# Performance work log

Hardware: AMD Instinct MI355X
Metric: run time of the kernel (lower is better)

Reference implementation:

```python
import jax, jax.numpy as jnp
import numpy as np

EPS = 1e-5

def _layer_norm(x, w, b):
    mu = jnp.mean(x, axis=-1, keepdims=True)
    var = jnp.mean(jnp.square(x - mu), axis=-1, keepdims=True)
    return (x - mu) * jax.lax.rsqrt(var + EPS) * w + b

def setup_inputs() -> dict:
    key = jax.random.key(0)
    ks = jax.random.split(key, 5)
    B, S, C = 1, 512, 128
    scale = 1.0 / np.sqrt(C)
    return {
        "z_ij": jax.random.normal(ks[0], (B, S, S, C), dtype=jnp.float32),
        "ln_w": jnp.ones((C,), jnp.float32),
        "ln_b": jnp.zeros((C,), jnp.float32),
        "wa": jax.random.normal(ks[1], (C, C), dtype=jnp.float32) * scale,
        "wb": jax.random.normal(ks[2], (C, C), dtype=jnp.float32) * scale,
        "wg": jax.random.normal(ks[3], (C, C), dtype=jnp.float32) * scale,
        "fln_w": jnp.ones((C,), jnp.float32),
        "fln_b": jnp.zeros((C,), jnp.float32),
        "wf": jax.random.normal(ks[4], (C, C), dtype=jnp.float32) * scale,
    }

def reference(z_ij, ln_w, ln_b, wa, wb, wg, fln_w, fln_b, wf):
    # z_ij: (B, S, S, C). torch Linear(x) == x @ W.T
    z = _layer_norm(z_ij, ln_w, ln_b)
    a = jax.nn.sigmoid(z @ wa.T)  # (B, S, S, C)
    b = jax.nn.sigmoid(z @ wb.T)
    g = jax.nn.sigmoid(z @ wg.T)
    # torch: einsum('...kic,...kjc->...ijc', a.transpose(-3,-2), b)
    # == out[i,j,c] = sum_k a[i,k,c] * b[k,j,c]
    p = jnp.einsum('bikc,bkjc->bijc', a, b)
    return g * (_layer_norm(p, fln_w, fln_b) @ wf.T)
```

## Files before the change

kernel.cpp:

```cpp
#include <hip/hip_runtime.h>

#define SS 512
#define CC 128
#define RR (SS*SS)

typedef unsigned short u16;
typedef unsigned int   u32;
typedef __attribute__((ext_vector_type(4))) float f32x4;
typedef __attribute__((ext_vector_type(8))) short s16x8;
typedef __attribute__((ext_vector_type(4))) u32   u32x4;

__device__ __forceinline__ float bf2f(u16 u){ u32 x = ((u32)u)<<16; float f; __builtin_memcpy(&f,&x,4); return f; }
__device__ __forceinline__ float sigf(float x){ return 1.f/(1.f + __expf(-x)); }

__device__ __forceinline__ u32 cvtpk(float lo, float hi){
  u32 r; asm("v_cvt_pk_bf16_f32 %0, %1, %2" : "=v"(r) : "v"(lo), "v"(hi)); return r;
}

typedef __attribute__((address_space(1))) void* gptr_t;
typedef __attribute__((address_space(3))) void* lptr_t;
__device__ __forceinline__ void load_lds16(const void* g, void* l){
  __builtin_amdgcn_global_load_lds((gptr_t)(g), (lptr_t)(l), 16, 0, 0);
}

__global__ void k0(const float* __restrict__ wa, const float* __restrict__ wb,
                   const float* __restrict__ wg, u16* __restrict__ wabg)
{
  int t = blockIdx.x*256 + threadIdx.x;
  const float* srcs[3] = {wa, wb, wg};
  int m = t >> 11;
  int e = (t & 2047) * 8;
  const float* s = srcs[m] + e;
  u32 pk[4];
  #pragma unroll
  for (int v=0; v<2; v++){
    f32x4 x = *reinterpret_cast<const f32x4*>(s + v*4);
    pk[v*2]   = cvtpk(x[0], x[1]);
    pk[v*2+1] = cvtpk(x[2], x[3]);
  }
  *reinterpret_cast<u32x4*>(wabg + m*16384 + e) = *reinterpret_cast<u32x4*>(pk);
}

__global__ __launch_bounds__(256,3) void k1(
    const float* __restrict__ z, const float* __restrict__ lnw, const float* __restrict__ lnb,
    const u16* __restrict__ wabg,
    u16* __restrict__ a_t, u16* __restrict__ b_t, u16* __restrict__ g_out,
    float* __restrict__ SaPart)
{
  __shared__ __align__(16) u16 zn[64][136];
  __shared__ __align__(16) u16 wk[64*128];
  __shared__ __align__(16) u16 tr[128*72];
  const int tid = threadIdx.x;
  const int r0  = blockIdx.x * 64;
  const int lane = tid & 63, w = tid >> 6;
  const int iI   = r0 >> 9;
  const int kblk = (r0 >> 6) & 7;

  auto stageW = [&](int m, int h){
    const u16* Wb = wabg + m*16384 + h*8192;
    #pragma unroll
    for (int s=0;s<4;s++){
      int lr = s*16 + (tid>>4);
      const u16* gsrc = Wb + lr*128 + (((tid&15) ^ (lr&7))<<3);
      load_lds16((const void*)gsrc, (void*)&wk[s*2048 + w*512]);
    }
  };

  stageW(0,0);

  {
    int row = tid >> 2, q = tid & 3;
    const float* src = z + (size_t)(r0+row)*CC + q*32;
    float v[32]; float s = 0.f, s2 = 0.f;
    #pragma unroll
    for (int i=0;i<8;i++){
      f32x4 t = *reinterpret_cast<const f32x4*>(src + i*4);
      #pragma unroll
      for (int e=0;e<4;e++){ float x = t[e]; v[i*4+e]=x; s += x; s2 += x*x; }
    }
    s  += __shfl_xor(s,1);  s2 += __shfl_xor(s2,1);
    s  += __shfl_xor(s,2);  s2 += __shfl_xor(s2,2);
    float mu  = s * (1.f/128.f);
    float var = s2*(1.f/128.f) - mu*mu;
    float rs  = rsqrtf(var + 1e-5f);
    #pragma unroll
    for (int i=0;i<4;i++){
      u32 pk[4];
      #pragma unroll
      for (int e=0;e<8;e+=2){
        int ci = i*8+e; int c = q*32 + ci;
        float y0 = (v[ci]  -mu)*rs*lnw[c]   + lnb[c];
        float y1 = (v[ci+1]-mu)*rs*lnw[c+1] + lnb[c+1];
        pk[e>>1] = cvtpk(y0, y1);
      }
      *reinterpret_cast<u32x4*>(&zn[row][q*32 + i*8]) = *reinterpret_cast<u32x4*>(pk);
    }
  }
  __syncthreads();

  s16x8 af[4];
  #pragma unroll
  for (int ks=0;ks<4;ks++)
    af[ks] = *reinterpret_cast<const s16x8*>(&zn[w*16 + (lane&15)][ks*32 + (lane>>4)*8]);

  for (int m=0;m<3;m++){
    f32x4 acc[8];
    #pragma unroll
    for (int cb=0;cb<8;cb++) acc[cb] = (f32x4){0.f,0.f,0.f,0.f};

    #pragma unroll
    for (int cb=0;cb<4;cb++){
      int lr = cb*16 + (lane&15);
      const int rx = (lr&7)<<3;
      const u16* base = &wk[lr*128];
      s16x8 b0 = *reinterpret_cast<const s16x8*>(&base[(  0 + (lane>>4)*8) ^ rx]);
      s16x8 b1 = *reinterpret_cast<const s16x8*>(&base[( 32 + (lane>>4)*8) ^ rx]);
      s16x8 b2 = *reinterpret_cast<const s16x8*>(&base[( 64 + (lane>>4)*8) ^ rx]);
      s16x8 b3 = *reinterpret_cast<const s16x8*>(&base[( 96 + (lane>>4)*8) ^ rx]);
      acc[cb] = __builtin_amdgcn_mfma_f32_16x16x32_bf16(af[0], b0, acc[cb], 0,0,0);
      acc[cb] = __builtin_amdgcn_mfma_f32_16x16x32_bf16(af[1], b1, acc[cb], 0,0,0);
      acc[cb] = __builtin_amdgcn_mfma_f32_16x16x32_bf16(af[2], b2, acc[cb], 0,0,0);
      acc[cb] = __builtin_amdgcn_mfma_f32_16x16x32_bf16(af[3], b3, acc[cb], 0,0,0);
    }
    __syncthreads();
    stageW(m,1);
    __syncthreads();

    #pragma unroll
    for (int cb=4;cb<8;cb++){
      int lr = (cb-4)*16 + (lane&15);
      const int rx = (lr&7)<<3;
      const u16* base = &wk[lr*128];
      s16x8 b0 = *reinterpret_cast<const s16x8*>(&base[(  0 + (lane>>4)*8) ^ rx]);
      s16x8 b1 = *reinterpret_cast<const s16x8*>(&base[( 32 + (lane>>4)*8) ^ rx]);
      s16x8 b2 = *reinterpret_cast<const s16x8*>(&base[( 64 + (lane>>4)*8) ^ rx]);
      s16x8 b3 = *reinterpret_cast<const s16x8*>(&base[( 96 + (lane>>4)*8) ^ rx]);
      acc[cb] = __builtin_amdgcn_mfma_f32_16x16x32_bf16(af[0], b0, acc[cb], 0,0,0);
      acc[cb] = __builtin_amdgcn_mfma_f32_16x16x32_bf16(af[1], b1, acc[cb], 0,0,0);
      acc[cb] = __builtin_amdgcn_mfma_f32_16x16x32_bf16(af[2], b2, acc[cb], 0,0,0);
      acc[cb] = __builtin_amdgcn_mfma_f32_16x16x32_bf16(af[3], b3, acc[cb], 0,0,0);
    }
    __syncthreads();

    if (m<2) stageW(m+1,0);

    if (m < 2){
      #pragma unroll
      for (int cb=0;cb<8;cb++){
        int col = cb*16 + (lane&15);
        int rbase = w*16 + (lane>>4)*4;
        u32 p0 = cvtpk(sigf(acc[cb][0])-0.5f, sigf(acc[cb][1])-0.5f);
        u32 p1 = cvtpk(sigf(acc[cb][2])-0.5f, sigf(acc[cb][3])-0.5f);
        u32* d = reinterpret_cast<u32*>(&tr[col*72 + rbase]);
        d[0] = p0; d[1] = p1;
      }
      asm volatile("s_waitcnt lgkmcnt(0)" ::: "memory");
      __builtin_amdgcn_s_barrier();
      {
        int c = tid>>1, half = tid&1;
        u16* dst = (m==0 ? a_t : b_t) + ((size_t)c<<18) + r0 + half*32;
        const u16* srcl = &tr[c*72 + half*32];
        float s = 0.f;
        #pragma unroll
        for (int e=0;e<4;e++){
          u32x4 t = *reinterpret_cast<const u32x4*>(srcl + e*8);
          *reinterpret_cast<u32x4*>(dst + e*8) = t;
          #pragma unroll
          for (int q=0;q<4;q++){ u32 v = t[q]; s += bf2f((u16)v) + bf2f((u16)(v>>16)); }
        }
        if (m==0){
          s += __shfl_xor(s, 1);
          if ((tid&1)==0) SaPart[(kblk<<16) + (iI<<7) + c] = s;
        }
      }
      __syncthreads();
    } else {
      u16* gb = &tr[0];
      #pragma unroll
      for (int cb=0;cb<8;cb++){
        int col = cb*16 + (lane&15);
        int rbase = w*16 + (lane>>4)*4;
        #pragma unroll
        for (int q=0;q<4;q++){
          float sg = sigf(acc[cb][q]);
          gb[(rbase+q)*136 + col] = (u16)cvtpk(sg, sg);
        }
      }
      asm volatile("s_waitcnt lgkmcnt(0)" ::: "memory");
      __builtin_amdgcn_s_barrier();
      {
        int row = tid>>2, qo = tid&3;
        u16* dst = g_out + (size_t)(r0+row)*CC + qo*32;
        const u16* srcl = &gb[row*136 + qo*32];
        #pragma unroll
        for (int e=0;e<4;e++)
          *reinterpret_cast<u32x4*>(dst + e*8) = *reinterpret_cast<const u32x4*>(srcl + e*8);
      }
    }
  }
}

__global__ __launch_bounds__(256,4) void k1b(const u16* __restrict__ b_t, u16* __restrict__ bT,
                                             float* __restrict__ SbPart)
{
  __shared__ __align__(16) u16 tile[64][72];
  const int tid = threadIdx.x;
  const int c  = blockIdx.x >> 6;
  const int t  = blockIdx.x & 63;
  const int k0 = (t>>3)*64, j0 = (t&7)*64;
  const u16* src = b_t + ((size_t)c<<18);
  {
    int row = tid>>3, chunk = tid&7;
    #pragma unroll
    for (int pass=0; pass<2; pass++){
      int k = row + pass*32;
      const u16* s = src + (size_t)(k0+k)*SS + j0 + chunk*8;
      u32x4 v = *reinterpret_cast<const u32x4*>(s);
      int cs = chunk ^ ((k>>3)&7);
      *reinterpret_cast<u32x4*>(&tile[k][cs*8]) = v;
    }
  }
  __syncthreads();
  {
    int j = tid>>2, part = tid&3;
    u32 pk[8];
    float sb = 0.f;
    #pragma unroll
    for (int i=0;i<16;i+=2){
      int ka = part*16 + i;
      int key = (ka>>3)&7;
      u16 va = tile[ka  ][(((j>>3)^key)*8) + (j&7)];
      u16 vb = tile[ka+1][(((j>>3)^key)*8) + (j&7)];
      pk[i>>1] = (u32)va | ((u32)vb<<16);
      sb += bf2f(va) + bf2f(vb);
    }
    u16* dst = bT + ((size_t)c<<18) + (size_t)(j0+j)*SS + k0 + part*16;
    *reinterpret_cast<u32x4*>(dst)   = *reinterpret_cast<u32x4*>(pk);
    *reinterpret_cast<u32x4*>(dst+8) = *reinterpret_cast<u32x4*>(pk+4);
    sb += __shfl_xor(sb, 1);
    sb += __shfl_xor(sb, 2);
    if (part==0) SbPart[(((c<<9) + j0 + j)<<3) + (k0>>6)] = sb;
  }
}

__global__ void k1c(const float* __restrict__ SaPart, const float* __restrict__ SbPart,
                    float* __restrict__ Sa, float* __restrict__ Sb)
{
  int idx = blockIdx.x*256 + threadIdx.x;
  if (idx < 65536){
    int i = idx >> 7, c = idx & 127;
    float s = 0.f;
    #pragma unroll
    for (int b=0;b<8;b++) s += SaPart[(b<<16) + (i<<7) + c];
    Sa[(c<<9) + i] = s;
  } else {
    int cj = idx & 65535;
    const float* src = SbPart + ((size_t)cj << 3);
    float s = 0.f;
    #pragma unroll
    for (int b=0;b<8;b++) s += src[b];
    Sb[cj] = s;
  }
}

__global__ __launch_bounds__(256,2) void k2(const u16* __restrict__ a_t, const u16* __restrict__ bT,
                                            const float* __restrict__ Sa, const float* __restrict__ Sb,
                                            _Float16* __restrict__ ph)
{
  __shared__ __align__(16) u16 As[2][128*64];
  __shared__ __align__(16) u16 Bs[128*64];
  const int tid = threadIdx.x;
  const int lane = tid & 63, w = tid >> 6;
  const int c  = blockIdx.y;
  const int i0 = (blockIdx.x >> 2) * 128, j0 = (blockIdx.x & 3) * 128;
  const u16* Ag = a_t + ((size_t)c<<18);
  const u16* Bg = bT  + ((size_t)c<<18);
  const int pr = lane>>3, slot = lane&7;

  auto stageA = [&](int kt, int buf){
    #pragma unroll
    for (int s=0;s<4;s++){
      int rbase = w*32 + s*8;
      int rl = rbase + pr;
      const u16* g = Ag + (size_t)(i0+rl)*SS + kt*64 + ((slot^pr)*8);
      load_lds16((const void*)g, (void*)&As[buf][rbase*64]);
    }
  };
  auto stageB = [&](int kt){
    #pragma unroll
    for (int s=0;s<4;s++){
      int rbase = w*32 + s*8;
      int rl = rbase + pr;
      const u16* g = Bg + (size_t)(j0+rl)*SS + kt*64 + ((slot^pr)*8);
      load_lds16((const void*)g, (void*)&Bs[rbase*64]);
    }
  };

  f32x4 acc[4][4];
  #pragma unroll
  for (int a=0;a<4;a++)
    #pragma unroll
    for (int b=0;b<4;b++) acc[a][b] = (f32x4){0.f,0.f,0.f,0.f};
  const int wr = w>>1, wc = w&1;

  stageA(0, 0);
  for (int kt=0; kt<8; ++kt){
    stageB(kt);
    if (kt < 7){
      stageA(kt+1, (kt+1)&1);
      asm volatile("s_waitcnt vmcnt(4)" ::: "memory");
    } else {
      asm volatile("s_waitcnt vmcnt(0)" ::: "memory");
    }
    __builtin_amdgcn_s_barrier();
    const u16* Ab = &As[kt&1][0];
    #pragma unroll
    for (int ks=0;ks<2;ks++){
      s16x8 af[4], bfv[4];
      #pragma unroll
      for (int f=0; f<4; f++){
        int i = wr*64 + f*16 + (lane&15);
        int ch = (ks*4 + (lane>>4)) ^ (i&7);
        af[f] = *reinterpret_cast<const s16x8*>(&Ab[i*64 + ch*8]);
        int j = wc*64 + f*16 + (lane&15);
        int chb = (ks*4 + (lane>>4)) ^ (j&7);
        bfv[f] = *reinterpret_cast<const s16x8*>(&Bs[j*64 + chb*8]);
      }
      #pragma unroll
      for (int fi=0;fi<4;fi++)
        #pragma unroll
        for (int fj=0;fj<4;fj++)
          acc[fi][fj] = __builtin_amdgcn_mfma_f32_16x16x32_bf16(af[fi], bfv[fj], acc[fi][fj], 0,0,0);
    }
    asm volatile("s_waitcnt lgkmcnt(0)" ::: "memory");
    __builtin_amdgcn_s_barrier();
  }

  _Float16* P = ph + ((size_t)c<<18);
  const float* SaC = Sa + (c<<9);
  const float* SbC = Sb + (c<<9);
  float sbv[4];
  #pragma unroll
  for (int fj=0;fj<4;fj++) sbv[fj] = SbC[j0 + wc*64 + fj*16 + (lane&15)];
  #pragma unroll
  for (int fi=0;fi<4;fi++){
    int rbase = i0 + wr*64 + fi*16 + (lane>>4)*4;
    #pragma unroll
    for (int q=0;q<4;q++){
      float sav = SaC[rbase+q];
      #pragma unroll
      for (int fj=0;fj<4;fj++){
        int col = j0 + wc*64 + fj*16 + (lane&15);
        P[(size_t)(rbase+q)*SS + col] = (_Float16)(0.5f*(sav + sbv[fj]) + acc[fi][fj][q]);
      }
    }
  }
}

__global__ __launch_bounds__(256,2) void k3(const _Float16* __restrict__ ph, const u16* __restrict__ g,
    const float* __restrict__ flnw, const float* __restrict__ flnb,
    const float* __restrict__ wf, float* __restrict__ out)
{
  __shared__ __align__(16) u16 znp[64][136];
  __shared__ __align__(16) u16 wk[128][136];
  __shared__ __align__(16) float red[4][64];
  __shared__ __align__(16) float muv[64], rsv[64];
  const int tid = threadIdx.x;
  const int rr0 = blockIdx.x * 64;
  const int lane = tid&63, w = tid>>6;
  const int pos = tid & 63, cq = tid >> 6;

  {
    int n = tid>>1, half = tid&1;
    const float* src = wf + n*CC + half*64;
    #pragma unroll
    for (int ch=0; ch<4; ch++){
      u32 pk[8];
      #pragma unroll
      for (int v4=0; v4<4; v4++){
        f32x4 t = *reinterpret_cast<const f32x4*>(src + ch*16 + v4*4);
        pk[v4*2]   = cvtpk(t[0], t[1]);
        pk[v4*2+1] = cvtpk(t[2], t[3]);
      }
      *reinterpret_cast<u32x4*>(&wk[n][half*64 + ch*16])     = *reinterpret_cast<u32x4*>(pk);
      *reinterpret_cast<u32x4*>(&wk[n][half*64 + ch*16 + 8]) = *reinterpret_cast<u32x4*>(pk+4);
    }
  }

  float pv[32];
  {
    const _Float16* src = ph + rr0 + pos;
    float s = 0.f;
    #pragma unroll
    for (int ci=0;ci<32;ci++){
      int c = cq*32 + ci;
      float x = (float)src[((size_t)c)<<18];
      pv[ci] = x; s += x;
    }
    red[cq][pos] = s;
  }
  __syncthreads();
  if (tid < 64) muv[tid] = (red[0][tid]+red[1][tid]+red[2][tid]+red[3][tid]) * (1.f/128.f);
  __syncthreads();
  float mu = muv[pos];
  {
    float s2 = 0.f;
    #pragma unroll
    for (int ci=0;ci<32;ci++){ float d = pv[ci]-mu; s2 += d*d; }
    red[cq][pos] = s2;
  }
  __syncthreads();
  if (tid < 64) rsv[tid] = rsqrtf((red[0][tid]+red[1][tid]+red[2][tid]+red[3][tid])*(1.f/128.f) + 1e-5f);
  __syncthreads();
  float rs = rsv[pos];
  {
    u32 pk[4];
    #pragma unroll
    for (int ii=0;ii<4;ii++){
      #pragma unroll
      for (int e=0;e<8;e+=2){
        int ci = ii*8+e; int c = cq*32+ci;
        float y0 = (pv[ci]  -mu)*rs*flnw[c]   + flnb[c];
        float y1 = (pv[ci+1]-mu)*rs*flnw[c+1] + flnb[c+1];
        pk[e>>1] = cvtpk(y0, y1);
      }
      *reinterpret_cast<u32x4*>(&znp[pos][cq*32 + ii*8]) = *reinterpret_cast<u32x4*>(pk);
    }
  }
  __syncthreads();

  f32x4 acc[8];
  #pragma unroll
  for (int cb=0;cb<8;cb++) acc[cb] = (f32x4){0.f,0.f,0.f,0.f};
  #pragma unroll
  for (int ks=0;ks<4;ks++){
    s16x8 af = *reinterpret_cast<const s16x8*>(&znp[w*16 + (lane&15)][ks*32 + (lane>>4)*8]);
    #pragma unroll
    for (int cb=0;cb<8;cb++){
      s16x8 bf = *reinterpret_cast<const s16x8*>(&wk[cb*16 + (lane&15)][ks*32 + (lane>>4)*8]);
      acc[cb] = __builtin_amdgcn_mfma_f32_16x16x32_bf16(af, bf, acc[cb], 0,0,0);
    }
  }
  __syncthreads();

  u16* gb = &znp[0][0];
  {
    int row = tid>>2, qo = tid&3;
    const u16* src = g + (size_t)(rr0+row)*CC + qo*32;
    #pragma unroll
    for (int e=0;e<4;e++)
      *reinterpret_cast<u32x4*>(&gb[row*136 + qo*32 + e*8]) = *reinterpret_cast<const u32x4*>(src + e*8);
  }
  __syncthreads();
  #pragma unroll
  for (int cb=0;cb<8;cb++){
    int col = cb*16 + (lane&15);
    int rbase = w*16 + (lane>>4)*4;
    #pragma unroll
    for (int q=0;q<4;q++){
      float gv = bf2f(gb[(rbase+q)*136 + col]);
      out[(size_t)(rr0+rbase+q)*CC + col] = gv * acc[cb][q];
    }
  }
}

extern "C" void kernel_launch(void* const* d_in, const int* in_sizes, int n_in,
                              void* d_out, int out_size, void* d_ws, size_t ws_size,
                              hipStream_t stream)
{
  const float* z    = (const float*)d_in[0];
  const float* lnw  = (const float*)d_in[1];
  const float* lnb  = (const float*)d_in[2];
  const float* wa   = (const float*)d_in[3];
  const float* wb   = (const float*)d_in[4];
  const float* wg   = (const float*)d_in[5];
  const float* flnw = (const float*)d_in[6];
  const float* flnb = (const float*)d_in[7];
  const float* wf   = (const float*)d_in[8];
  float* out = (float*)d_out;

  char* ws = (char*)d_ws;
  u16* a_t = (u16*)(ws);
  u16* bT  = (u16*)(ws + ((size_t)64<<20));
  u16* g   = (u16*)(ws + ((size_t)128<<20));
  _Float16* ph = (_Float16*)(ws + ((size_t)192<<20));
  u16* b_t = (u16*)(ws + ((size_t)192<<20));

  char* ob = (char*)d_out;
  u16*   wabg   = (u16*)ob;
  float* SaPart = (float*)(ob + ((size_t)1<<20));
  float* SbPart = (float*)(ob + ((size_t)3<<20));
  float* Sa     = (float*)(ob + ((size_t)5<<20));
  float* Sb     = (float*)(ob + ((size_t)5<<20) + ((size_t)256<<10));

  k0 <<<24,   256, 0, stream>>>(wa, wb, wg, wabg);
  k1 <<<4096, 256, 0, stream>>>(z, lnw, lnb, wabg, a_t, b_t, g, SaPart);
  k1b<<<8192, 256, 0, stream>>>(b_t, bT, SbPart);
  k1c<<<512,  256, 0, stream>>>(SaPart, SbPart, Sa, Sb);
  k2 <<<dim3(16,128), 256, 0, stream>>>(a_t, bT, Sa, Sb, ph);
  k3 <<<4096, 256, 0, stream>>>(ph, g, flnw, flnb, wf, out);
}
```

Before: 316.2 us.

## Pre-convert wf once, alias k1 LDS buffers, swizzle k2 grid, raise occupancy

The wf weight is now converted to bf16 once in k0, and k3 loads it into swizzled LDS with direct global-to-LDS loads. Before, every k3 block converted the fp32 weight itself. k1 now shares one LDS buffer for the zn and tr arrays so its launch bound can go from 3 to 4 blocks, and k3's bound goes from 2 to 3. k2 switches to a 1D grid with a block-index swizzle that changes which channel and tile blocks run together, likely for cache locality. Aliasing zn and tr is only correct if the hidden k1 code separates their uses with barriers, and the higher occupancy targets may cause register spills.

```diff
diff --git a/kernel.cpp b/kernel.cpp
--- a/kernel.cpp
+++ b/kernel.cpp
@@ -24,10 +24,11 @@
 }
 
 __global__ void k0(const float* __restrict__ wa, const float* __restrict__ wb,
-                   const float* __restrict__ wg, u16* __restrict__ wabg)
+                   const float* __restrict__ wg, const float* __restrict__ wf,
+                   u16* __restrict__ wabg, u16* __restrict__ wfbg)
 {
   int t = blockIdx.x*256 + threadIdx.x;
-  const float* srcs[3] = {wa, wb, wg};
+  const float* srcs[4] = {wa, wb, wg, wf};
   int m = t >> 11;
   int e = (t & 2047) * 8;
   const float* s = srcs[m] + e;
@@ -38,18 +39,20 @@
     pk[v*2]   = cvtpk(x[0], x[1]);
     pk[v*2+1] = cvtpk(x[2], x[3]);
   }
-  *reinterpret_cast<u32x4*>(wabg + m*16384 + e) = *reinterpret_cast<u32x4*>(pk);
-}
-
-__global__ __launch_bounds__(256,3) void k1(
+  u16* dst = (m==3) ? (wfbg + e) : (wabg + m*16384 + e);
+  *reinterpret_cast<u32x4*>(dst) = *reinterpret_cast<u32x4*>(pk);
+}
+
+__global__ __launch_bounds__(256,4) void k1(
     const float* __restrict__ z, const float* __restrict__ lnw, const float* __restrict__ lnb,
     const u16* __restrict__ wabg,
     u16* __restrict__ a_t, u16* __restrict__ b_t, u16* __restrict__ g_out,
     float* __restrict__ SaPart)
 {
-  __shared__ __align__(16) u16 zn[64][136];
+  __shared__ __align__(16) u16 un[9216];
   __shared__ __align__(16) u16 wk[64*128];
-  __shared__ __align__(16) u16 tr[128*72];
+  u16 (*zn)[136] = reinterpret_cast<u16(*)[136]>(un);
+  u16* tr = un;
   const int tid = threadIdx.x;
   const int r0  = blockIdx.x * 64;
   const int lane = tid & 63, w = tid >> 6;
@@ -271,8 +274,11 @@
   __shared__ __align__(16) u16 Bs[128*64];
   const int tid = threadIdx.x;
   const int lane = tid & 63, w = tid >> 6;
-  const int c  = blockIdx.y;
-  const int i0 = (blockIdx.x >> 2) * 128, j0 = (blockIdx.x & 3) * 128;
+  const int bid = blockIdx.x;
+  const int swz = (bid & 7) * 256 + (bid >> 3);
+  const int c   = swz >> 4;
+  const int t16 = swz & 15;
+  const int i0 = (t16 >> 2) * 128, j0 = (t16 & 3) * 128;
   const u16* Ag = a_t + ((size_t)c<<18);
   const u16* Bg = bT  + ((size_t)c<<18);
   const int pr = lane>>3, slot = lane&7;
@@ -357,12 +363,12 @@
   }
 }
 
-__global__ __launch_bounds__(256,2) void k3(const _Float16* __restrict__ ph, const u16* __restrict__ g,
+__global__ __launch_bounds__(256,3) void k3(const _Float16* __restrict__ ph, const u16* __restrict__ g,
     const float* __restrict__ flnw, const float* __restrict__ flnb,
-    const float* __restrict__ wf, float* __restrict__ out)
+    const u16* __restrict__ wfbg, float* __restrict__ out)
 {
   __shared__ __align__(16) u16 znp[64][136];
-  __shared__ __align__(16) u16 wk[128][136];
+  __shared__ __align__(16) u16 wk[128*128];
   __shared__ __align__(16) float red[4][64];
   __shared__ __align__(16) float muv[64], rsv[64];
   const int tid = threadIdx.x;
@@ -371,19 +377,11 @@
   const int pos = tid & 63, cq = tid >> 6;
 
   {
-    int n = tid>>1, half = tid&1;
-    const float* src = wf + n*CC + half*64;
-    #pragma unroll
-    for (int ch=0; ch<4; ch++){
-      u32 pk[8];
-      #pragma unroll
-      for (int v4=0; v4<4; v4++){
-        f32x4 t = *reinterpret_cast<const f32x4*>(src + ch*16 + v4*4);
-        pk[v4*2]   = cvtpk(t[0], t[1]);
-        pk[v4*2+1] = cvtpk(t[2], t[3]);
-      }
-      *reinterpret_cast<u32x4*>(&wk[n][half*64 + ch*16])     = *reinterpret_cast<u32x4*>(pk);
-      *reinterpret_cast<u32x4*>(&wk[n][half*64 + ch*16 + 8]) = *reinterpret_cast<u32x4*>(pk+4);
+    #pragma unroll
+    for (int s=0;s<8;s++){
+      int row = s*16 + (tid>>4);
+      const u16* gsrc = wfbg + row*128 + (((tid&15) ^ (row&7))<<3);
+      load_lds16((const void*)gsrc, (void*)&wk[s*2048 + w*512]);
     }
   }
 
@@ -437,7 +435,9 @@
     s16x8 af = *reinterpret_cast<const s16x8*>(&znp[w*16 + (lane&15)][ks*32 + (lane>>4)*8]);
     #pragma unroll
     for (int cb=0;cb<8;cb++){
-      s16x8 bf = *reinterpret_cast<const s16x8*>(&wk[cb*16 + (lane&15)][ks*32 + (lane>>4)*8]);
+      int row = cb*16 + (lane&15);
+      const int rx = (row&7)<<3;
+      s16x8 bf = *reinterpret_cast<const s16x8*>(&wk[row*128 + ((ks*32 + (lane>>4)*8) ^ rx)]);
       acc[cb] = __builtin_amdgcn_mfma_f32_16x16x32_bf16(af, bf, acc[cb], 0,0,0);
     }
   }
@@ -485,6 +485,7 @@
   u16* g   = (u16*)(ws + ((size_t)128<<20));
   _Float16* ph = (_Float16*)(ws + ((size_t)192<<20));
   u16* b_t = (u16*)(ws + ((size_t)192<<20));
+  u16* wfbg = (u16*)(ws + ((size_t)256<<20));
 
   char* ob = (char*)d_out;
   u16*   wabg   = (u16*)ob;
@@ -493,10 +494,10 @@
   float* Sa     = (float*)(ob + ((size_t)5<<20));
   float* Sb     = (float*)(ob + ((size_t)5<<20) + ((size_t)256<<10));
 
-  k0 <<<24,   256, 0, stream>>>(wa, wb, wg, wabg);
+  k0 <<<32,   256, 0, stream>>>(wa, wb, wg, wf, wabg, wfbg);
   k1 <<<4096, 256, 0, stream>>>(z, lnw, lnb, wabg, a_t, b_t, g, SaPart);
   k1b<<<8192, 256, 0, stream>>>(b_t, bT, SbPart);
   k1c<<<512,  256, 0, stream>>>(SaPart, SbPart, Sa, Sb);
-  k2 <<<dim3(16,128), 256, 0, stream>>>(a_t, bT, Sa, Sb, ph);
-  k3 <<<4096, 256, 0, stream>>>(ph, g, flnw, flnb, wf, out);
-}
+  k2 <<<2048, 256, 0, stream>>>(a_t, bT, Sa, Sb, ph);
+  k3 <<<4096, 256, 0, stream>>>(ph, g, flnw, flnb, wfbg, out);
+}
```

Result: faster. 276.6 us (-12.5%).
